# Kernel tuning notes

Hardware: AMD Instinct MI355X
Metric: run time of the kernel (lower is better)

## Reference

```python
import jax, jax.numpy as jnp
import numpy as np

N_NODES = 100_000
N_EDGES = 1_600_000
NUM_GRAPHS = 512
D1, D2, D3, D5, NUM_CLASSES = 3, 50, 15, 10, 6
BN_EPS = 1e-5


def setup_inputs() -> dict:
    key = jax.random.key(0)
    ks = jax.random.split(key, 16)

    def w(k, shape):
        fan_in = shape[0]
        return jax.random.normal(k, shape, jnp.float32) / np.sqrt(fan_in).astype(np.float32)

    return {
        "x": jax.random.normal(ks[0], (N_NODES, D1), jnp.float32),
        "edge_attr": jax.random.normal(ks[1], (N_EDGES, D1), jnp.float32),
        # edge MLP: Lin(9,50) -> ReLU -> Lin(50,15)
        "edge_w1": w(ks[2], (3 * D1, D2)), "edge_b1": jnp.zeros((D2,), jnp.float32),
        "edge_w2": w(ks[3], (D2, D3)), "edge_b2": jnp.zeros((D3,), jnp.float32),
        # node MLP: Lin(18,50) -> ReLU -> Lin(50,15)
        "node_w1": w(ks[4], (D1 + D3, D2)), "node_b1": jnp.zeros((D2,), jnp.float32),
        "node_w2": w(ks[5], (D2, D3)), "node_b2": jnp.zeros((D3,), jnp.float32),
        # readout head
        "fc1_w": w(ks[6], (D3, D5)), "fc1_b": jnp.zeros((D5,), jnp.float32),
        "bn_gamma": jnp.ones((D5,), jnp.float32), "bn_beta": jnp.zeros((D5,), jnp.float32),
        "fc2_w": w(ks[7], (D5, NUM_CLASSES)), "fc2_b": jnp.zeros((NUM_CLASSES,), jnp.float32),
        # graph structure
        "edge_index": jax.random.randint(ks[8], (2, N_EDGES), 0, N_NODES, jnp.int32),
        "batch": jnp.sort(jax.random.randint(ks[9], (N_NODES,), 0, NUM_GRAPHS, jnp.int32)),
    }


def _segment_mean(vals, idx, num_segments):
    s = jax.ops.segment_sum(vals, idx, num_segments=num_segments)
    c = jax.ops.segment_sum(jnp.ones((vals.shape[0], 1), vals.dtype), idx,
                            num_segments=num_segments)
    return s / jnp.maximum(c, 1.0)


def reference(x, edge_attr,
              edge_w1, edge_b1, edge_w2, edge_b2,
              node_w1, node_b1, node_w2, node_b2,
              fc1_w, fc1_b, bn_gamma, bn_beta, fc2_w, fc2_b,
              edge_index, batch):
    row, col = edge_index[0], edge_index[1]
    # edge model: cat([x[row], x[col], edge_attr]) -> MLP  -> [E, D3]
    e_in = jnp.concatenate([x[row], x[col], edge_attr], axis=1)
    edge_attr2 = jax.nn.relu(e_in @ edge_w1 + edge_b1) @ edge_w2 + edge_b2
    # node model: cat([x[col], edge_attr2]) -> MLP -> scatter_mean over row
    n_in = jnp.concatenate([x[col], edge_attr2], axis=1)  # [E, D1+D3]
    msg = jax.nn.relu(n_in @ node_w1 + node_b1) @ node_w2 + node_b2  # [E, D3]
    x2 = _segment_mean(msg, row, x.shape[0])  # [N, D3]
    # global mean pool per graph -> [G, D3]
    u = _segment_mean(x2, batch, NUM_GRAPHS)
    # head: fc1 -> BatchNorm1d (batch stats) -> relu -> fc2 -> log_softmax
    h = u @ fc1_w + fc1_b
    mu = h.mean(axis=0)
    var = h.var(axis=0)  # biased, matches BN training normalization
    h = bn_gamma * (h - mu) * jax.lax.rsqrt(var + BN_EPS) + bn_beta
    h = jax.nn.relu(h)
    logits = h @ fc2_w + fc2_b
    return jax.nn.log_softmax(logits, axis=1)
```

## Files before the change

### kernel.cpp

```cpp
#include <hip/hip_runtime.h>
#include <hip/hip_bf16.h>
#include <math.h>

#define N_NODES    100000
#define N_EDGES    1600000
#define NUM_GRAPHS 512
#define D2 50
#define D3 15
#define D5 10
#define NCLS 6
#define BN_EPS 1e-5f

#define NBLK1 ((N_NODES + 1023) / 1024)

#define W_EW1T 0
#define W_EW2T 2560
#define W_NW1T 3712
#define W_NW2T 6272
#define W_TOTAL 7680

#define S_EIN  40
#define S_HB   104
#define ACT_WAVE 2944

typedef __attribute__((ext_vector_type(8))) short short8;
typedef __attribute__((ext_vector_type(4))) float float4_;

__device__ __forceinline__ unsigned short f2bf(float f) {
    __hip_bfloat16 h = __float2bfloat16(f);
    union { __hip_bfloat16 h; unsigned short u; } c; c.h = h; return c.u;
}
__device__ __forceinline__ float bf2f(unsigned short u) {
    union { __hip_bfloat16 h; unsigned short u; } c; c.u = u;
    return __bfloat162float(c.h);
}
__device__ __forceinline__ unsigned int pkbf(float a, float b) {
    return (unsigned int)f2bf(a) | ((unsigned int)f2bf(b) << 16);
}

__global__ __launch_bounds__(256) void prep_kernel(
    const float* __restrict__ ew1, const float* __restrict__ eb1,
    const float* __restrict__ ew2, const float* __restrict__ eb2,
    const float* __restrict__ nw1, const float* __restrict__ nb1,
    const float* __restrict__ nw2, const float* __restrict__ nb2,
    unsigned short* __restrict__ wh, unsigned short* __restrict__ wl,
    const float* __restrict__ x, ushort4* __restrict__ x4b,
    const int* __restrict__ edge_index, int* __restrict__ counts)
{
    int gtid = blockIdx.x * 256 + threadIdx.x;
    int gsz = gridDim.x * 256;

    for (int i = gtid; i < W_TOTAL; i += gsz) {
        float v = 0.0f;
        if (i < W_EW2T) {
            int m = i / 40, k = i % 40;
            if (m < 50) {
                if (k < 3)                 v = ew1[k * 50 + m];
                else if (k == 3)           v = eb1[m];
                else if (k >= 4 && k < 7)  v = ew1[(k - 1) * 50 + m];
                else if (k >= 8 && k < 11) v = ew1[(k - 2) * 50 + m];
            }
        } else if (i < W_NW1T) {
            int j = i - W_EW2T; int m = j / 72, k = j % 72;
            if (m < 15) { if (k < 50) v = ew2[k * 15 + m]; else if (k == 50) v = eb2[m]; }
        } else if (i < W_NW2T) {
            int j = i - W_NW1T; int m = j / 40, k = j % 40;
            if (m < 50) {
                if (k < 15)                  v = nw1[(3 + k) * 50 + m];
                else if (k >= 16 && k < 19)  v = nw1[(k - 16) * 50 + m];
                else if (k == 19)            v = nb1[m];
            }
        } else if (i < 7424) {
            int j = i - W_NW2T; int m = j / 72, k = j % 72;
            if (m < 15) { if (k < 50) v = nw2[k * 15 + m]; else if (k == 50) v = nb2[m]; }
        }
        unsigned short h = f2bf(v);
        unsigned short l = f2bf(v - bf2f(h));
        wh[i] = h; wl[i] = l;
    }

    for (int n = gtid; n < N_NODES; n += gsz) {
        ushort4 v;
        v.x = f2bf(x[n * 3 + 0]); v.y = f2bf(x[n * 3 + 1]);
        v.z = f2bf(x[n * 3 + 2]); v.w = 0;
        x4b[n] = v;
    }

    for (int e = gtid; e < N_EDGES; e += gsz)
        atomicAdd(&counts[edge_index[e]], 1);
}

__global__ __launch_bounds__(1024) void scan1_kernel(
    const int* __restrict__ counts, int* __restrict__ scanned, int* __restrict__ bsums)
{
    __shared__ int tmp[1024];
    int i = blockIdx.x * 1024 + threadIdx.x;
    int v = (i < N_NODES) ? counts[i] : 0;
    tmp[threadIdx.x] = v;
    __syncthreads();
    #pragma unroll
    for (int off = 1; off < 1024; off <<= 1) {
        int t = (threadIdx.x >= off) ? tmp[threadIdx.x - off] : 0;
        __syncthreads();
        tmp[threadIdx.x] += t;
        __syncthreads();
    }
    int incl = tmp[threadIdx.x];
    if (i < N_NODES) scanned[i] = incl - v;
    if (threadIdx.x == 1023) bsums[blockIdx.x] = incl;
}

__global__ __launch_bounds__(128) void scan2_kernel(
    const int* __restrict__ bsums, int* __restrict__ bofs)
{
    __shared__ int tmp[128];
    int v = (threadIdx.x < NBLK1) ? bsums[threadIdx.x] : 0;
    tmp[threadIdx.x] = v;
    __syncthreads();
    #pragma unroll
    for (int off = 1; off < 128; off <<= 1) {
        int t = (threadIdx.x >= off) ? tmp[threadIdx.x - off] : 0;
        __syncthreads();
        tmp[threadIdx.x] += t;
        __syncthreads();
    }
    if (threadIdx.x < NBLK1) bofs[threadIdx.x] = tmp[threadIdx.x] - v;
}

__global__ __launch_bounds__(256) void scan3_kernel(
    const int* __restrict__ scanned, const int* __restrict__ bofs,
    int* __restrict__ cursor)
{
    int n = blockIdx.x * 256 + threadIdx.x;
    if (n >= N_NODES) return;
    cursor[n] = scanned[n] + bofs[n >> 10];
}

__global__ __launch_bounds__(256) void edge_mfma_kernel(
    const unsigned short* __restrict__ wh_g, const unsigned short* __restrict__ wl_g,
    const ushort4* __restrict__ x4b, const float* __restrict__ edge_attr,
    const int* __restrict__ edge_index,
    int* __restrict__ cursor, float* __restrict__ msg)
{
    __shared__ unsigned short act[4][ACT_WAVE];

    int tid = threadIdx.x, wave = tid >> 6, lane = tid & 63;
    int t16 = lane & 15, quad = lane >> 4;
    unsigned short* ein  = &act[wave][0];
    unsigned short* hbuf = &act[wave][640];
    unsigned short* h2in = &act[wave][2304];

    short8 A1h[4], A1l[4], A3h[4], A3l[4];
    #pragma unroll
    for (int t4 = 0; t4 < 4; t4++) {
        int o1 = W_EW1T + (t4 * 16 + t16) * 40 + quad * 8;
        A1h[t4] = *(const short8*)(wh_g + o1);
        A1l[t4] = *(const short8*)(wl_g + o1);
        int o3 = W_NW1T + (t4 * 16 + t16) * 40 + quad * 8;
        A3h[t4] = *(const short8*)(wh_g + o3);
        A3l[t4] = *(const short8*)(wl_g + o3);
    }
    short8 A2h[2], A2l[2], A4h[2], A4l[2];
    #pragma unroll
    for (int kc = 0; kc < 2; kc++) {
        int o2 = W_EW2T + t16 * 72 + kc * 32 + quad * 8;
        A2h[kc] = *(const short8*)(wh_g + o2);
        A2l[kc] = *(const short8*)(wl_g + o2);
        int o4 = W_NW2T + t16 * 72 + kc * 32 + quad * 8;
        A4h[kc] = *(const short8*)(wh_g + o4);
        A4l[kc] = *(const short8*)(wl_g + o4);
    }

    ushort4 z4; z4.x = 0; z4.y = 0; z4.z = 0; z4.w = 0;
    for (int i = lane; i < 16 * 5; i += 64) {
        int r = i / 5, c = i % 5;
        *(ushort4*)&ein[r * S_EIN + 12 + c * 4] = z4;
    }
    for (int i = lane; i < 16 * 3; i += 64) {
        int r = i / 3, c = i % 3;
        *(ushort4*)&h2in[r * S_EIN + 20 + c * 4] = z4;
    }
    __builtin_amdgcn_wave_barrier();

    int gw = blockIdx.x * 4 + wave;
    for (int t = gw; t < N_EDGES / 16; t += 4000) {
        int e = t * 16 + t16;
        int pos = 0;
        if (quad == 0) {
            int row = edge_index[e];
            ushort4 xr = x4b[row];
            ushort4 w; w.x = xr.x; w.y = xr.y; w.z = xr.z; w.w = 0x3F80;
            *(ushort4*)&ein[t16 * S_EIN + 0] = w;
            pos = atomicAdd(&cursor[row], 1);
        } else if (quad == 1) {
            int col = edge_index[N_EDGES + e];
            ushort4 xc = x4b[col];
            *(ushort4*)&ein[t16 * S_EIN + 4] = xc;
        } else if (quad == 2) {
            ushort4 w;
            w.x = f2bf(edge_attr[e * 3 + 0]);
            w.y = f2bf(edge_attr[e * 3 + 1]);
            w.z = f2bf(edge_attr[e * 3 + 2]);
            w.w = 0;
            *(ushort4*)&ein[t16 * S_EIN + 8] = w;
        } else {
            int col = edge_index[N_EDGES + e];
            ushort4 xc = x4b[col];
            ushort4 w; w.x = xc.x; w.y = xc.y; w.z = xc.z; w.w = 0x3F80;
            *(ushort4*)&h2in[t16 * S_EIN + 16] = w;
        }
        pos = __shfl(pos, t16);
        __builtin_amdgcn_wave_barrier();

        short8 B1 = *(short8*)&ein[t16 * S_EIN + quad * 8];
        #pragma unroll
        for (int t4 = 0; t4 < 4; t4++) {
            float4_ z = {0.f, 0.f, 0.f, 0.f};
            z = __builtin_amdgcn_mfma_f32_16x16x32_bf16(A1l[t4], B1, z, 0, 0, 0);
            z = __builtin_amdgcn_mfma_f32_16x16x32_bf16(A1h[t4], B1, z, 0, 0, 0);
            float r0 = fmaxf(z[0], 0.f), r1 = fmaxf(z[1], 0.f);
            float r2 = fmaxf(z[2], 0.f), r3 = fmaxf(z[3], 0.f);
            uint2 pk; pk.x = pkbf(r0, r1); pk.y = pkbf(r2, r3);
            *(uint2*)&hbuf[t16 * S_HB + t4 * 16 + quad * 4] = pk;
        }
        if (quad == 0) hbuf[t16 * S_HB + 50] = 0x3F80;
        __builtin_amdgcn_wave_barrier();

        float4_ acc2 = {0.f, 0.f, 0.f, 0.f};
        #pragma unroll
        for (int kc = 0; kc < 2; kc++) {
            short8 B = *(short8*)&hbuf[t16 * S_HB + kc * 32 + quad * 8];
            acc2 = __builtin_amdgcn_mfma_f32_16x16x32_bf16(A2l[kc], B, acc2, 0, 0, 0);
            acc2 = __builtin_amdgcn_mfma_f32_16x16x32_bf16(A2h[kc], B, acc2, 0, 0, 0);
        }
        {
            uint2 pk; pk.x = pkbf(acc2[0], acc2[1]); pk.y = pkbf(acc2[2], acc2[3]);
            *(uint2*)&h2in[t16 * S_EIN + quad * 4] = pk;
        }
        __builtin_amdgcn_wave_barrier();

        short8 B3 = *(short8*)&h2in[t16 * S_EIN + quad * 8];
        #pragma unroll
        for (int t4 = 0; t4 < 4; t4++) {
            float4_ z = {0.f, 0.f, 0.f, 0.f};
            z = __builtin_amdgcn_mfma_f32_16x16x32_bf16(A3l[t4], B3, z, 0, 0, 0);
            z = __builtin_amdgcn_mfma_f32_16x16x32_bf16(A3h[t4], B3, z, 0, 0, 0);
            float r0 = fmaxf(z[0], 0.f), r1 = fmaxf(z[1], 0.f);
            float r2 = fmaxf(z[2], 0.f), r3 = fmaxf(z[3], 0.f);
            uint2 pk; pk.x = pkbf(r0, r1); pk.y = pkbf(r2, r3);
            *(uint2*)&hbuf[t16 * S_HB + t4 * 16 + quad * 4] = pk;
        }
        if (quad == 0) hbuf[t16 * S_HB + 50] = 0x3F80;
        __builtin_amdgcn_wave_barrier();

        float4_ accm = {0.f, 0.f, 0.f, 0.f};
        #pragma unroll
        for (int kc = 0; kc < 2; kc++) {
            short8 B = *(short8*)&hbuf[t16 * S_HB + kc * 32 + quad * 8];
            accm = __builtin_amdgcn_mfma_f32_16x16x32_bf16(A4l[kc], B, accm, 0, 0, 0);
            accm = __builtin_amdgcn_mfma_f32_16x16x32_bf16(A4h[kc], B, accm, 0, 0, 0);
        }
        *(float4_*)(msg + (size_t)pos * 16 + quad * 4) = accm;
        __builtin_amdgcn_wave_barrier();
    }
}

__global__ __launch_bounds__(256) void gather_pool_kernel(
    const float* __restrict__ msg, const int* __restrict__ scanned,
    const int* __restrict__ bofs, const int* __restrict__ counts,
    const int* __restrict__ batch, float* __restrict__ gsum)
{
    __shared__ float acc[64 * 16];
    int n0 = blockIdx.x * 256;
    int n = n0 + threadIdx.x;

    float v[16];
    #pragma unroll
    for (int k = 0; k < 16; k++) v[k] = 0.0f;
    if (n < N_NODES) {
        int start = scanned[n] + bofs[n >> 10];
        int deg = counts[n];
        for (int j = 0; j < deg; j++) {
            const float4* mp = (const float4*)(msg + (size_t)(start + j) * 16);
            float4 b0 = mp[0], b1 = mp[1], b2 = mp[2], b3 = mp[3];
            v[0] += b0.x;  v[1] += b0.y;  v[2] += b0.z;  v[3] += b0.w;
            v[4] += b1.x;  v[5] += b1.y;  v[6] += b1.z;  v[7] += b1.w;
            v[8] += b2.x;  v[9] += b2.y;  v[10] += b2.z; v[11] += b2.w;
            v[12] += b3.x; v[13] += b3.y; v[14] += b3.z;
        }
        float inv = 1.0f / fmaxf((float)deg, 1.0f);
        #pragma unroll
        for (int k = 0; k < 15; k++) v[k] *= inv;
        v[15] = 1.0f;
    }

    int gmin = batch[n0];
    int gmax = batch[min(n0 + 255, N_NODES - 1)];
    int range = gmax - gmin + 1;
    if (range <= 64) {
        for (int t = threadIdx.x; t < range * 16; t += 256) acc[t] = 0.0f;
        __syncthreads();
        if (n < N_NODES) {
            int g = batch[n] - gmin;
            float* dst = &acc[g * 16];
            #pragma unroll
            for (int k = 0; k < 16; k++) atomicAdd(&dst[k], v[k]);
        }
        __syncthreads();
        for (int t = threadIdx.x; t < range * 16; t += 256) {
            float w = acc[t];
            if (w != 0.0f) atomicAdd(&gsum[(size_t)gmin * 16 + t], w);
        }
    } else {
        if (n < N_NODES) {
            int g = batch[n];
            float* dst = gsum + (size_t)g * 16;
            #pragma unroll
            for (int k = 0; k < 16; k++) atomicAdd(&dst[k], v[k]);
        }
    }
}

__global__ __launch_bounds__(512) void head_kernel(
    const float* __restrict__ gsum,
    const float* __restrict__ fc1w, const float* __restrict__ fc1b,
    const float* __restrict__ gamma, const float* __restrict__ beta,
    const float* __restrict__ fc2w, const float* __restrict__ fc2b,
    float* __restrict__ out)
{
    __shared__ float ssum[D5], ssq[D5], smu[D5], sistd[D5];
    int g = threadIdx.x;
    if (g < D5) { ssum[g] = 0.0f; ssq[g] = 0.0f; }
    __syncthreads();

    const float* src = gsum + (size_t)g * 16;
    float inv = 1.0f / fmaxf(src[15], 1.0f);
    float u[D3];
    #pragma unroll
    for (int k = 0; k < D3; k++) u[k] = src[k] * inv;

    float h[D5];
    #pragma unroll
    for (int c = 0; c < D5; c++) h[c] = fc1b[c];
    #pragma unroll
    for (int k = 0; k < D3; k++) {
        float v = u[k];
        #pragma unroll
        for (int c = 0; c < D5; c++) h[c] = fmaf(v, fc1w[k * D5 + c], h[c]);
    }

    int lane = threadIdx.x & 63;
    #pragma unroll
    for (int c = 0; c < D5; c++) {
        float v = h[c];
        float v2 = v * v;
        #pragma unroll
        for (int off = 32; off >= 1; off >>= 1) {
            v  += __shfl_xor(v,  off);
            v2 += __shfl_xor(v2, off);
        }
        if (lane == 0) { atomicAdd(&ssum[c], v); atomicAdd(&ssq[c], v2); }
    }
    __syncthreads();
    if (g < D5) {
        float mu = ssum[g] * (1.0f / NUM_GRAPHS);
        float var = ssq[g] * (1.0f / NUM_GRAPHS) - mu * mu;
        smu[g] = mu;
        sistd[g] = rsqrtf(var + BN_EPS);
    }
    __syncthreads();

    float hn[D5];
    #pragma unroll
    for (int c = 0; c < D5; c++) {
        float v = gamma[c] * (h[c] - smu[c]) * sistd[c] + beta[c];
        hn[c] = fmaxf(v, 0.0f);
    }

    float lg[NCLS];
    #pragma unroll
    for (int j = 0; j < NCLS; j++) lg[j] = fc2b[j];
    #pragma unroll
    for (int c = 0; c < D5; c++) {
        float v = hn[c];
        #pragma unroll
        for (int j = 0; j < NCLS; j++) lg[j] = fmaf(v, fc2w[c * NCLS + j], lg[j]);
    }

    float m = lg[0];
    #pragma unroll
    for (int j = 1; j < NCLS; j++) m = fmaxf(m, lg[j]);
    float se = 0.0f;
    #pragma unroll
    for (int j = 0; j < NCLS; j++) se += expf(lg[j] - m);
    float lse = logf(se);
    #pragma unroll
    for (int j = 0; j < NCLS; j++) out[g * NCLS + j] = lg[j] - m - lse;
}

extern "C" void kernel_launch(void* const* d_in, const int* in_sizes, int n_in,
                              void* d_out, int out_size, void* d_ws, size_t ws_size,
                              hipStream_t stream) {
    const float* x         = (const float*)d_in[0];
    const float* edge_attr = (const float*)d_in[1];
    const float* ew1  = (const float*)d_in[2];
    const float* eb1  = (const float*)d_in[3];
    const float* ew2  = (const float*)d_in[4];
    const float* eb2  = (const float*)d_in[5];
    const float* nw1  = (const float*)d_in[6];
    const float* nb1  = (const float*)d_in[7];
    const float* nw2  = (const float*)d_in[8];
    const float* nb2  = (const float*)d_in[9];
    const float* fc1w = (const float*)d_in[10];
    const float* fc1b = (const float*)d_in[11];
    const float* gamma= (const float*)d_in[12];
    const float* beta = (const float*)d_in[13];
    const float* fc2w = (const float*)d_in[14];
    const float* fc2b = (const float*)d_in[15];
    const int* edge_index = (const int*)d_in[16];
    const int* batch      = (const int*)d_in[17];

    char* p = (char*)d_ws;
    float* msg = (float*)p;            p += (size_t)N_EDGES * 16 * sizeof(float);
    int* counts  = (int*)p;            p += (size_t)N_NODES * sizeof(int);
    int* scanned = (int*)p;            p += (size_t)N_NODES * sizeof(int);
    int* cursor  = (int*)p;            p += (size_t)N_NODES * sizeof(int);
    int* bsums   = (int*)p;            p += 128 * sizeof(int);
    int* bofs    = (int*)p;            p += 128 * sizeof(int);
    ushort4* x4b = (ushort4*)p;        p += (size_t)N_NODES * sizeof(ushort4);
    float* gsum  = (float*)p;          p += (size_t)NUM_GRAPHS * 16 * sizeof(float);
    unsigned short* wh = (unsigned short*)p; p += W_TOTAL * sizeof(unsigned short);
    unsigned short* wl = (unsigned short*)p; p += W_TOTAL * sizeof(unsigned short);

    hipMemsetAsync(counts, 0, (size_t)N_NODES * sizeof(int), stream);
    hipMemsetAsync(gsum, 0, (size_t)NUM_GRAPHS * 16 * sizeof(float), stream);

    int egrid = (N_EDGES + 255) / 256;
    int ngrid = (N_NODES + 255) / 256;

    prep_kernel<<<egrid, 256, 0, stream>>>(
        ew1, eb1, ew2, eb2, nw1, nb1, nw2, nb2, wh, wl,
        x, x4b, edge_index, counts);
    scan1_kernel<<<NBLK1, 1024, 0, stream>>>(counts, scanned, bsums);
    scan2_kernel<<<1, 128, 0, stream>>>(bsums, bofs);
    scan3_kernel<<<ngrid, 256, 0, stream>>>(scanned, bofs, cursor);
    edge_mfma_kernel<<<1000, 256, 0, stream>>>(
        wh, wl, x4b, edge_attr, edge_index, cursor, msg);
    gather_pool_kernel<<<ngrid, 256, 0, stream>>>(
        msg, scanned, bofs, counts, batch, gsum);
    head_kernel<<<1, 512, 0, stream>>>(
        gsum, fc1w, fc1b, gamma, beta, fc2w, fc2b, (float*)d_out);
}
```

Baseline: 382.4 us.

## Software-pipeline edge loads and process two 16-edge tiles per wave iteration

The edge MLP kernel now handles two 16-edge tiles per iteration with double LDS buffers, interleaving independent MFMA chains so they can hide each other's latency. The gathers and cursor atomics for the next pair of tiles are issued before the current tiles' MFMA work, overlapping memory latency with compute. The grid grows from 1000 to 2500 blocks with a fixed iteration count (50000 tiles / 10000 waves = 5). LDS per block doubles and register pressure rises, which may lower occupancy.

```diff
diff --git a/kernel.cpp b/kernel.cpp
--- a/kernel.cpp
+++ b/kernel.cpp
@@ -21,7 +21,12 @@
 
 #define S_EIN  40
 #define S_HB   104
-#define ACT_WAVE 2944
+#define ACT_WAVE 5888
+
+#define EDGE_BLOCKS 2500
+#define EDGE_WAVES  (EDGE_BLOCKS * 4)
+#define TILES32     (N_EDGES / 32)
+#define EDGE_ITERS  (TILES32 / EDGE_WAVES)
 
 typedef __attribute__((ext_vector_type(8))) short short8;
 typedef __attribute__((ext_vector_type(4))) float float4_;
@@ -136,6 +141,38 @@
     cursor[n] = scanned[n] + bofs[n >> 10];
 }
 
+__device__ __forceinline__ void load_stage(int e, int quad,
+    const int* __restrict__ edge_index, const ushort4* __restrict__ x4b,
+    const float* __restrict__ edge_attr, int* __restrict__ cursor,
+    ushort4& w, int& pos)
+{
+    if (quad == 0) {
+        int row = edge_index[e];
+        ushort4 xr = x4b[row];
+        w.x = xr.x; w.y = xr.y; w.z = xr.z; w.w = 0x3F80;
+        pos = atomicAdd(&cursor[row], 1);
+    } else if (quad == 1) {
+        int col = edge_index[N_EDGES + e];
+        w = x4b[col];
+    } else if (quad == 2) {
+        w.x = f2bf(edge_attr[e * 3 + 0]);
+        w.y = f2bf(edge_attr[e * 3 + 1]);
+        w.z = f2bf(edge_attr[e * 3 + 2]);
+        w.w = 0;
+    } else {
+        int col = edge_index[N_EDGES + e];
+        ushort4 xc = x4b[col];
+        w.x = xc.x; w.y = xc.y; w.z = xc.z; w.w = 0x3F80;
+    }
+}
+
+__device__ __forceinline__ void write_stage(
+    unsigned short* ein, unsigned short* h2in, int t16, int quad, ushort4 w)
+{
+    if (quad < 3) *(ushort4*)&ein[t16 * S_EIN + quad * 4] = w;
+    else          *(ushort4*)&h2in[t16 * S_EIN + 16] = w;
+}
+
 __global__ __launch_bounds__(256) void edge_mfma_kernel(
     const unsigned short* __restrict__ wh_g, const unsigned short* __restrict__ wl_g,
     const ushort4* __restrict__ x4b, const float* __restrict__ edge_attr,
@@ -146,9 +183,13 @@
 
     int tid = threadIdx.x, wave = tid >> 6, lane = tid & 63;
     int t16 = lane & 15, quad = lane >> 4;
-    unsigned short* ein  = &act[wave][0];
-    unsigned short* hbuf = &act[wave][640];
-    unsigned short* h2in = &act[wave][2304];
+    unsigned short* base = act[wave];
+    unsigned short* einA = base;
+    unsigned short* einB = base + 640;
+    unsigned short* h2A  = base + 1280;
+    unsigned short* h2B  = base + 1920;
+    unsigned short* hbA  = base + 2560;
+    unsigned short* hbB  = base + 4224;
 
     short8 A1h[4], A1l[4], A3h[4], A3l[4];
     #pragma unroll
@@ -174,94 +215,116 @@
     ushort4 z4; z4.x = 0; z4.y = 0; z4.z = 0; z4.w = 0;
     for (int i = lane; i < 16 * 5; i += 64) {
         int r = i / 5, c = i % 5;
-        *(ushort4*)&ein[r * S_EIN + 12 + c * 4] = z4;
+        *(ushort4*)&einA[r * S_EIN + 12 + c * 4] = z4;
+        *(ushort4*)&einB[r * S_EIN + 12 + c * 4] = z4;
     }
     for (int i = lane; i < 16 * 3; i += 64) {
         int r = i / 3, c = i % 3;
-        *(ushort4*)&h2in[r * S_EIN + 20 + c * 4] = z4;
+        *(ushort4*)&h2A[r * S_EIN + 20 + c * 4] = z4;
+        *(ushort4*)&h2B[r * S_EIN + 20 + c * 4] = z4;
     }
     __builtin_amdgcn_wave_barrier();
 
     int gw = blockIdx.x * 4 + wave;
-    for (int t = gw; t < N_EDGES / 16; t += 4000) {
-        int e = t * 16 + t16;
-        int pos = 0;
+    int t = gw;
+    ushort4 wA, wB; int posA = 0, posB = 0;
+    load_stage(t * 32 + t16,      quad, edge_index, x4b, edge_attr, cursor, wA, posA);
+    load_stage(t * 32 + 16 + t16, quad, edge_index, x4b, edge_attr, cursor, wB, posB);
+
+    for (int it = 0; it < EDGE_ITERS; it++) {
+        write_stage(einA, h2A, t16, quad, wA);
+        write_stage(einB, h2B, t16, quad, wB);
+        int p0 = __shfl(posA, t16);
+        int p1 = __shfl(posB, t16);
+        __builtin_amdgcn_wave_barrier();
+
+        int tn = t + EDGE_WAVES;
+        ushort4 nA = z4, nB = z4; int nposA = 0, nposB = 0;
+        if (it + 1 < EDGE_ITERS) {
+            load_stage(tn * 32 + t16,      quad, edge_index, x4b, edge_attr, cursor, nA, nposA);
+            load_stage(tn * 32 + 16 + t16, quad, edge_index, x4b, edge_attr, cursor, nB, nposB);
+        }
+
+        short8 B1a = *(short8*)&einA[t16 * S_EIN + quad * 8];
+        short8 B1b = *(short8*)&einB[t16 * S_EIN + quad * 8];
+        #pragma unroll
+        for (int t4 = 0; t4 < 4; t4++) {
+            float4_ zA = {0.f, 0.f, 0.f, 0.f}, zB = {0.f, 0.f, 0.f, 0.f};
+            zA = __builtin_amdgcn_mfma_f32_16x16x32_bf16(A1l[t4], B1a, zA, 0, 0, 0);
+            zB = __builtin_amdgcn_mfma_f32_16x16x32_bf16(A1l[t4], B1b, zB, 0, 0, 0);
+            zA = __builtin_amdgcn_mfma_f32_16x16x32_bf16(A1h[t4], B1a, zA, 0, 0, 0);
+            zB = __builtin_amdgcn_mfma_f32_16x16x32_bf16(A1h[t4], B1b, zB, 0, 0, 0);
+            uint2 pA, pB;
+            pA.x = pkbf(fmaxf(zA[0], 0.f), fmaxf(zA[1], 0.f));
+            pA.y = pkbf(fmaxf(zA[2], 0.f), fmaxf(zA[3], 0.f));
+            pB.x = pkbf(fmaxf(zB[0], 0.f), fmaxf(zB[1], 0.f));
+            pB.y = pkbf(fmaxf(zB[2], 0.f), fmaxf(zB[3], 0.f));
+            *(uint2*)&hbA[t16 * S_HB + t4 * 16 + quad * 4] = pA;
+            *(uint2*)&hbB[t16 * S_HB + t4 * 16 + quad * 4] = pB;
+        }
         if (quad == 0) {
-            int row = edge_index[e];
-            ushort4 xr = x4b[row];
-            ushort4 w; w.x = xr.x; w.y = xr.y; w.z = xr.z; w.w = 0x3F80;
-            *(ushort4*)&ein[t16 * S_EIN + 0] = w;
-            pos = atomicAdd(&cursor[row], 1);
-        } else if (quad == 1) {
-            int col = edge_index[N_EDGES + e];
-            ushort4 xc = x4b[col];
-            *(ushort4*)&ein[t16 * S_EIN + 4] = xc;
-        } else if (quad == 2) {
-            ushort4 w;
-            w.x = f2bf(edge_attr[e * 3 + 0]);
-            w.y = f2bf(edge_attr[e * 3 + 1]);
-            w.z = f2bf(edge_attr[e * 3 + 2]);
-            w.w = 0;
-            *(ushort4*)&ein[t16 * S_EIN + 8] = w;
-        } else {
-            int col = edge_index[N_EDGES + e];
-            ushort4 xc = x4b[col];
-            ushort4 w; w.x = xc.x; w.y = xc.y; w.z = xc.z; w.w = 0x3F80;
-            *(ushort4*)&h2in[t16 * S_EIN + 16] = w;
-        }
-        pos = __shfl(pos, t16);
+            hbA[t16 * S_HB + 50] = 0x3F80;
+            hbB[t16 * S_HB + 50] = 0x3F80;
+        }
         __builtin_amdgcn_wave_barrier();
 
-        short8 B1 = *(short8*)&ein[t16 * S_EIN + quad * 8];
+        float4_ a2A = {0.f, 0.f, 0.f, 0.f}, a2B = {0.f, 0.f, 0.f, 0.f};
+        #pragma unroll
+        for (int kc = 0; kc < 2; kc++) {
+            short8 BA = *(short8*)&hbA[t16 * S_HB + kc * 32 + quad * 8];
+            short8 BB = *(short8*)&hbB[t16 * S_HB + kc * 32 + quad * 8];
+            a2A = __builtin_amdgcn_mfma_f32_16x16x32_bf16(A2l[kc], BA, a2A, 0, 0, 0);
+            a2B = __builtin_amdgcn_mfma_f32_16x16x32_bf16(A2l[kc], BB, a2B, 0, 0, 0);
+            a2A = __builtin_amdgcn_mfma_f32_16x16x32_bf16(A2h[kc], BA, a2A, 0, 0, 0);
+            a2B = __builtin_amdgcn_mfma_f32_16x16x32_bf16(A2h[kc], BB, a2B, 0, 0, 0);
+        }
+        {
+            uint2 pA, pB;
+            pA.x = pkbf(a2A[0], a2A[1]); pA.y = pkbf(a2A[2], a2A[3]);
+            pB.x = pkbf(a2B[0], a2B[1]); pB.y = pkbf(a2B[2], a2B[3]);
+            *(uint2*)&h2A[t16 * S_EIN + quad * 4] = pA;
+            *(uint2*)&h2B[t16 * S_EIN + quad * 4] = pB;
+        }
+        __builtin_amdgcn_wave_barrier();
+
+        short8 B3a = *(short8*)&h2A[t16 * S_EIN + quad * 8];
+        short8 B3b = *(short8*)&h2B[t16 * S_EIN + quad * 8];
         #pragma unroll
         for (int t4 = 0; t4 < 4; t4++) {
-            float4_ z = {0.f, 0.f, 0.f, 0.f};
-            z = __builtin_amdgcn_mfma_f32_16x16x32_bf16(A1l[t4], B1, z, 0, 0, 0);
-            z = __builtin_amdgcn_mfma_f32_16x16x32_bf16(A1h[t4], B1, z, 0, 0, 0);
-            float r0 = fmaxf(z[0], 0.f), r1 = fmaxf(z[1], 0.f);
-            float r2 = fmaxf(z[2], 0.f), r3 = fmaxf(z[3], 0.f);
-            uint2 pk; pk.x = pkbf(r0, r1); pk.y = pkbf(r2, r3);
-            *(uint2*)&hbuf[t16 * S_HB + t4 * 16 + quad * 4] = pk;
-        }
-        if (quad == 0) hbuf[t16 * S_HB + 50] = 0x3F80;
+            float4_ zA = {0.f, 0.f, 0.f, 0.f}, zB = {0.f, 0.f, 0.f, 0.f};
+            zA = __builtin_amdgcn_mfma_f32_16x16x32_bf16(A3l[t4], B3a, zA, 0, 0, 0);
+            zB = __builtin_amdgcn_mfma_f32_16x16x32_bf16(A3l[t4], B3b, zB, 0, 0, 0);
+            zA = __builtin_amdgcn_mfma_f32_16x16x32_bf16(A3h[t4], B3a, zA, 0, 0, 0);
+            zB = __builtin_amdgcn_mfma_f32_16x16x32_bf16(A3h[t4], B3b, zB, 0, 0, 0);
+            uint2 pA, pB;
+            pA.x = pkbf(fmaxf(zA[0], 0.f), fmaxf(zA[1], 0.f));
+            pA.y = pkbf(fmaxf(zA[2], 0.f), fmaxf(zA[3], 0.f));
+            pB.x = pkbf(fmaxf(zB[0], 0.f), fmaxf(zB[1], 0.f));
+            pB.y = pkbf(fmaxf(zB[2], 0.f), fmaxf(zB[3], 0.f));
+            *(uint2*)&hbA[t16 * S_HB + t4 * 16 + quad * 4] = pA;
+            *(uint2*)&hbB[t16 * S_HB + t4 * 16 + quad * 4] = pB;
+        }
+        if (quad == 0) {
+            hbA[t16 * S_HB + 50] = 0x3F80;
+            hbB[t16 * S_HB + 50] = 0x3F80;
+        }
         __builtin_amdgcn_wave_barrier();
 
-        float4_ acc2 = {0.f, 0.f, 0.f, 0.f};
+        float4_ mA = {0.f, 0.f, 0.f, 0.f}, mB = {0.f, 0.f, 0.f, 0.f};
         #pragma unroll
         for (int kc = 0; kc < 2; kc++) {
-            short8 B = *(short8*)&hbuf[t16 * S_HB + kc * 32 + quad * 8];
-            acc2 = __builtin_amdgcn_mfma_f32_16x16x32_bf16(A2l[kc], B, acc2, 0, 0, 0);
-            acc2 = __builtin_amdgcn_mfma_f32_16x16x32_bf16(A2h[kc], B, acc2, 0, 0, 0);
-        }
-        {
-            uint2 pk; pk.x = pkbf(acc2[0], acc2[1]); pk.y = pkbf(acc2[2], acc2[3]);
-            *(uint2*)&h2in[t16 * S_EIN + quad * 4] = pk;
-        }
+            short8 BA = *(short8*)&hbA[t16 * S_HB + kc * 32 + quad * 8];
+            short8 BB = *(short8*)&hbB[t16 * S_HB + kc * 32 + quad * 8];
+            mA = __builtin_amdgcn_mfma_f32_16x16x32_bf16(A4l[kc], BA, mA, 0, 0, 0);
+            mB = __builtin_amdgcn_mfma_f32_16x16x32_bf16(A4l[kc], BB, mB, 0, 0, 0);
+            mA = __builtin_amdgcn_mfma_f32_16x16x32_bf16(A4h[kc], BA, mA, 0, 0, 0);
+            mB = __builtin_amdgcn_mfma_f32_16x16x32_bf16(A4h[kc], BB, mB, 0, 0, 0);
+        }
+        *(float4_*)(msg + (size_t)p0 * 16 + quad * 4) = mA;
+        *(float4_*)(msg + (size_t)p1 * 16 + quad * 4) = mB;
         __builtin_amdgcn_wave_barrier();
 
-        short8 B3 = *(short8*)&h2in[t16 * S_EIN + quad * 8];
-        #pragma unroll
-        for (int t4 = 0; t4 < 4; t4++) {
-            float4_ z = {0.f, 0.f, 0.f, 0.f};
-            z = __builtin_amdgcn_mfma_f32_16x16x32_bf16(A3l[t4], B3, z, 0, 0, 0);
-            z = __builtin_amdgcn_mfma_f32_16x16x32_bf16(A3h[t4], B3, z, 0, 0, 0);
-            float r0 = fmaxf(z[0], 0.f), r1 = fmaxf(z[1], 0.f);
-            float r2 = fmaxf(z[2], 0.f), r3 = fmaxf(z[3], 0.f);
-            uint2 pk; pk.x = pkbf(r0, r1); pk.y = pkbf(r2, r3);
-            *(uint2*)&hbuf[t16 * S_HB + t4 * 16 + quad * 4] = pk;
-        }
-        if (quad == 0) hbuf[t16 * S_HB + 50] = 0x3F80;
-        __builtin_amdgcn_wave_barrier();
-
-        float4_ accm = {0.f, 0.f, 0.f, 0.f};
-        #pragma unroll
-        for (int kc = 0; kc < 2; kc++) {
-            short8 B = *(short8*)&hbuf[t16 * S_HB + kc * 32 + quad * 8];
-            accm = __builtin_amdgcn_mfma_f32_16x16x32_bf16(A4l[kc], B, accm, 0, 0, 0);
-            accm = __builtin_amdgcn_mfma_f32_16x16x32_bf16(A4h[kc], B, accm, 0, 0, 0);
-        }
-        *(float4_*)(msg + (size_t)pos * 16 + quad * 4) = accm;
-        __builtin_amdgcn_wave_barrier();
+        wA = nA; wB = nB; posA = nposA; posB = nposB; t = tn;
     }
 }
 
@@ -444,7 +507,7 @@
     scan1_kernel<<<NBLK1, 1024, 0, stream>>>(counts, scanned, bsums);
     scan2_kernel<<<1, 128, 0, stream>>>(bsums, bofs);
     scan3_kernel<<<ngrid, 256, 0, stream>>>(scanned, bofs, cursor);
-    edge_mfma_kernel<<<1000, 256, 0, stream>>>(
+    edge_mfma_kernel<<<EDGE_BLOCKS, 256, 0, stream>>>(
         wh, wl, x4b, edge_attr, edge_index, cursor, msg);
     gather_pool_kernel<<<ngrid, 256, 0, stream>>>(
         msg, scanned, bofs, counts, batch, gsum);
```

Result: faster. 358.0 us (-6.4%).

## Replace LDS staging with bpermute register shuffles, process two edge tiles with prefetch

Applied to the files above, without the earlier changes.

The edge MLP kernel no longer stages activations through shared memory. It moves MFMA outputs into B-operand layout with ds_bpermute cross-lane shuffles. Each wave now handles two 16-edge tiles per iteration, interleaving their MFMAs to hide latency, and software-prefetches the next iteration's gathers and cursor atomics. The grid grows to 2500 blocks so the 32-edge tiles divide evenly. This raises register pressure and adds many bpermute instructions, and the input encoding is packed differently, which could break correctness if the lane mapping is wrong.

```diff
diff --git a/kernel.cpp b/kernel.cpp
--- a/kernel.cpp
+++ b/kernel.cpp
@@ -19,12 +19,14 @@
 #define W_NW2T 6272
 #define W_TOTAL 7680
 
-#define S_EIN  40
-#define S_HB   104
-#define ACT_WAVE 2944
+#define EDGE_BLOCKS 2500
+#define EDGE_WAVES  (EDGE_BLOCKS * 4)
+#define TILES32     (N_EDGES / 32)
+#define EDGE_ITERS  (TILES32 / EDGE_WAVES)
 
 typedef __attribute__((ext_vector_type(8))) short short8;
 typedef __attribute__((ext_vector_type(4))) float float4_;
+union BU { unsigned u[4]; short8 s; };
 
 __device__ __forceinline__ unsigned short f2bf(float f) {
     __hip_bfloat16 h = __float2bfloat16(f);
@@ -36,6 +38,9 @@
 }
 __device__ __forceinline__ unsigned int pkbf(float a, float b) {
     return (unsigned int)f2bf(a) | ((unsigned int)f2bf(b) << 16);
+}
+__device__ __forceinline__ unsigned bp(int s4, unsigned v) {
+    return (unsigned)__builtin_amdgcn_ds_bpermute(s4, (int)v);
 }
 
 __global__ __launch_bounds__(256) void prep_kernel(
@@ -136,132 +141,210 @@
     cursor[n] = scanned[n] + bofs[n >> 10];
 }
 
+struct EIn { unsigned w0, w1, w2, w3, h0, h1; int pos; };
+
+__device__ __forceinline__ EIn load_in(int ebase, int n, int quad,
+    const int* __restrict__ edge_index, const ushort4* __restrict__ x4b,
+    const float* __restrict__ edge_attr, int* __restrict__ cursor)
+{
+    EIn r; r.w0 = r.w1 = r.w2 = r.w3 = 0; r.h0 = r.h1 = 0; r.pos = 0;
+    int e = ebase + n;
+    if (quad == 0) {
+        int row = edge_index[e];
+        int col = edge_index[N_EDGES + e];
+        ushort4 xr = x4b[row];
+        ushort4 xc = x4b[col];
+        r.w0 = (unsigned)xr.x | ((unsigned)xr.y << 16);
+        r.w1 = (unsigned)xr.z | (0x3F80u << 16);
+        r.w2 = (unsigned)xc.x | ((unsigned)xc.y << 16);
+        r.w3 = (unsigned)xc.z;
+        r.pos = atomicAdd(&cursor[row], 1);
+    } else if (quad == 1) {
+        r.w0 = pkbf(edge_attr[e * 3 + 0], edge_attr[e * 3 + 1]);
+        r.w1 = (unsigned)f2bf(edge_attr[e * 3 + 2]);
+    } else if (quad == 2) {
+        int col = edge_index[N_EDGES + e];
+        ushort4 xc = x4b[col];
+        r.h0 = (unsigned)xc.x | ((unsigned)xc.y << 16);
+        r.h1 = (unsigned)xc.z | (0x3F80u << 16);
+    }
+    return r;
+}
+
+__device__ __forceinline__ void perm64(const unsigned U[4][2], int s0, int s1, bool hi,
+                                       short8& Bc0, short8& Bc1)
+{
+    BU b0, b1;
+    {
+        unsigned a0 = bp(s0, U[0][0]), a1 = bp(s0, U[1][0]);
+        unsigned a2 = bp(s0, U[0][1]), a3 = bp(s0, U[1][1]);
+        unsigned a4 = bp(s1, U[0][0]), a5 = bp(s1, U[1][0]);
+        unsigned a6 = bp(s1, U[0][1]), a7 = bp(s1, U[1][1]);
+        b0.u[0] = hi ? a1 : a0;
+        b0.u[1] = hi ? a3 : a2;
+        b0.u[2] = hi ? a5 : a4;
+        b0.u[3] = hi ? a7 : a6;
+    }
+    {
+        unsigned a0 = bp(s0, U[2][0]), a1 = bp(s0, U[3][0]);
+        unsigned a2 = bp(s0, U[2][1]), a3 = bp(s0, U[3][1]);
+        unsigned a4 = bp(s1, U[2][0]), a5 = bp(s1, U[3][0]);
+        unsigned a6 = bp(s1, U[2][1]), a7 = bp(s1, U[3][1]);
+        b1.u[0] = hi ? a1 : a0;
+        b1.u[1] = hi ? a3 : a2;
+        b1.u[2] = hi ? a5 : a4;
+        b1.u[3] = hi ? a7 : a6;
+    }
+    Bc0 = b0.s; Bc1 = b1.s;
+}
+
+__device__ __forceinline__ short8 perm16(const unsigned U2[2], int s0, int s1,
+                                         int quad, unsigned h0, unsigned h1)
+{
+    BU d;
+    d.u[0] = bp(s0, U2[0]);
+    d.u[1] = bp(s0, U2[1]);
+    d.u[2] = bp(s1, U2[0]);
+    d.u[3] = bp(s1, U2[1]);
+    if (quad == 2) { d.u[0] = h0; d.u[1] = h1; d.u[2] = 0; d.u[3] = 0; }
+    else if (quad == 3) { d.u[0] = 0; d.u[1] = 0; d.u[2] = 0; d.u[3] = 0; }
+    return d.s;
+}
+
 __global__ __launch_bounds__(256) void edge_mfma_kernel(
     const unsigned short* __restrict__ wh_g, const unsigned short* __restrict__ wl_g,
     const ushort4* __restrict__ x4b, const float* __restrict__ edge_attr,
     const int* __restrict__ edge_index,
     int* __restrict__ cursor, float* __restrict__ msg)
 {
-    __shared__ unsigned short act[4][ACT_WAVE];
-
     int tid = threadIdx.x, wave = tid >> 6, lane = tid & 63;
-    int t16 = lane & 15, quad = lane >> 4;
-    unsigned short* ein  = &act[wave][0];
-    unsigned short* hbuf = &act[wave][640];
-    unsigned short* h2in = &act[wave][2304];
+    int n = lane & 15, quad = lane >> 4;
 
     short8 A1h[4], A1l[4], A3h[4], A3l[4];
     #pragma unroll
     for (int t4 = 0; t4 < 4; t4++) {
-        int o1 = W_EW1T + (t4 * 16 + t16) * 40 + quad * 8;
+        int o1 = W_EW1T + (t4 * 16 + n) * 40 + quad * 8;
         A1h[t4] = *(const short8*)(wh_g + o1);
         A1l[t4] = *(const short8*)(wl_g + o1);
-        int o3 = W_NW1T + (t4 * 16 + t16) * 40 + quad * 8;
+        int o3 = W_NW1T + (t4 * 16 + n) * 40 + quad * 8;
         A3h[t4] = *(const short8*)(wh_g + o3);
         A3l[t4] = *(const short8*)(wl_g + o3);
     }
     short8 A2h[2], A2l[2], A4h[2], A4l[2];
     #pragma unroll
     for (int kc = 0; kc < 2; kc++) {
-        int o2 = W_EW2T + t16 * 72 + kc * 32 + quad * 8;
+        int o2 = W_EW2T + n * 72 + kc * 32 + quad * 8;
         A2h[kc] = *(const short8*)(wh_g + o2);
         A2l[kc] = *(const short8*)(wl_g + o2);
-        int o4 = W_NW2T + t16 * 72 + kc * 32 + quad * 8;
+        int o4 = W_NW2T + n * 72 + kc * 32 + quad * 8;
         A4h[kc] = *(const short8*)(wh_g + o4);
         A4l[kc] = *(const short8*)(wl_g + o4);
     }
 
-    ushort4 z4; z4.x = 0; z4.y = 0; z4.z = 0; z4.w = 0;
-    for (int i = lane; i < 16 * 5; i += 64) {
-        int r = i / 5, c = i % 5;
-        *(ushort4*)&ein[r * S_EIN + 12 + c * 4] = z4;
-    }
-    for (int i = lane; i < 16 * 3; i += 64) {
-        int r = i / 3, c = i % 3;
-        *(ushort4*)&h2in[r * S_EIN + 20 + c * 4] = z4;
-    }
-    __builtin_amdgcn_wave_barrier();
-
-    int gw = blockIdx.x * 4 + wave;
-    for (int t = gw; t < N_EDGES / 16; t += 4000) {
-        int e = t * 16 + t16;
-        int pos = 0;
-        if (quad == 0) {
-            int row = edge_index[e];
-            ushort4 xr = x4b[row];
-            ushort4 w; w.x = xr.x; w.y = xr.y; w.z = xr.z; w.w = 0x3F80;
-            *(ushort4*)&ein[t16 * S_EIN + 0] = w;
-            pos = atomicAdd(&cursor[row], 1);
-        } else if (quad == 1) {
-            int col = edge_index[N_EDGES + e];
-            ushort4 xc = x4b[col];
-            *(ushort4*)&ein[t16 * S_EIN + 4] = xc;
-        } else if (quad == 2) {
-            ushort4 w;
-            w.x = f2bf(edge_attr[e * 3 + 0]);
-            w.y = f2bf(edge_attr[e * 3 + 1]);
-            w.z = f2bf(edge_attr[e * 3 + 2]);
-            w.w = 0;
-            *(ushort4*)&ein[t16 * S_EIN + 8] = w;
-        } else {
-            int col = edge_index[N_EDGES + e];
-            ushort4 xc = x4b[col];
-            ushort4 w; w.x = xc.x; w.y = xc.y; w.z = xc.z; w.w = 0x3F80;
-            *(ushort4*)&h2in[t16 * S_EIN + 16] = w;
-        }
-        pos = __shfl(pos, t16);
-        __builtin_amdgcn_wave_barrier();
-
-        short8 B1 = *(short8*)&ein[t16 * S_EIN + quad * 8];
+    int s0 = ((quad & 1) * 32 + n) * 4;
+    int s1 = s0 + 64;
+    bool hi = (quad & 2) != 0;
+
+    int t = blockIdx.x * 4 + wave;
+    EIn cur0 = load_in(t * 32,      n, quad, edge_index, x4b, edge_attr, cursor);
+    EIn cur1 = load_in(t * 32 + 16, n, quad, edge_index, x4b, edge_attr, cursor);
+
+    for (int it = 0; it < EDGE_ITERS; it++) {
+        int p0 = __shfl(cur0.pos, n);
+        int p1 = __shfl(cur1.pos, n);
+
+        int tn = t + EDGE_WAVES;
+        EIn nx0, nx1;
+        nx0.w0 = nx0.w1 = nx0.w2 = nx0.w3 = nx0.h0 = nx0.h1 = 0; nx0.pos = 0;
+        nx1 = nx0;
+        if (it + 1 < EDGE_ITERS) {
+            nx0 = load_in(tn * 32,      n, quad, edge_index, x4b, edge_attr, cursor);
+            nx1 = load_in(tn * 32 + 16, n, quad, edge_index, x4b, edge_attr, cursor);
+        }
+
+        BU t0, t1;
+        t0.u[0] = cur0.w0; t0.u[1] = cur0.w1; t0.u[2] = cur0.w2; t0.u[3] = cur0.w3;
+        t1.u[0] = cur1.w0; t1.u[1] = cur1.w1; t1.u[2] = cur1.w2; t1.u[3] = cur1.w3;
+        short8 B1a = t0.s, B1b = t1.s;
+
+        unsigned U1a[4][2], U1b[4][2];
         #pragma unroll
         for (int t4 = 0; t4 < 4; t4++) {
-            float4_ z = {0.f, 0.f, 0.f, 0.f};
-            z = __builtin_amdgcn_mfma_f32_16x16x32_bf16(A1l[t4], B1, z, 0, 0, 0);
-            z = __builtin_amdgcn_mfma_f32_16x16x32_bf16(A1h[t4], B1, z, 0, 0, 0);
-            float r0 = fmaxf(z[0], 0.f), r1 = fmaxf(z[1], 0.f);
-            float r2 = fmaxf(z[2], 0.f), r3 = fmaxf(z[3], 0.f);
-            uint2 pk; pk.x = pkbf(r0, r1); pk.y = pkbf(r2, r3);
-            *(uint2*)&hbuf[t16 * S_HB + t4 * 16 + quad * 4] = pk;
-        }
-        if (quad == 0) hbuf[t16 * S_HB + 50] = 0x3F80;
-        __builtin_amdgcn_wave_barrier();
-
-        float4_ acc2 = {0.f, 0.f, 0.f, 0.f};
-        #pragma unroll
-        for (int kc = 0; kc < 2; kc++) {
-            short8 B = *(short8*)&hbuf[t16 * S_HB + kc * 32 + quad * 8];
-            acc2 = __builtin_amdgcn_mfma_f32_16x16x32_bf16(A2l[kc], B, acc2, 0, 0, 0);
-            acc2 = __builtin_amdgcn_mfma_f32_16x16x32_bf16(A2h[kc], B, acc2, 0, 0, 0);
-        }
-        {
-            uint2 pk; pk.x = pkbf(acc2[0], acc2[1]); pk.y = pkbf(acc2[2], acc2[3]);
-            *(uint2*)&h2in[t16 * S_EIN + quad * 4] = pk;
-        }
-        __builtin_amdgcn_wave_barrier();
-
-        short8 B3 = *(short8*)&h2in[t16 * S_EIN + quad * 8];
+            float4_ za = {0.f, 0.f, 0.f, 0.f}, zb = {0.f, 0.f, 0.f, 0.f};
+            za = __builtin_amdgcn_mfma_f32_16x16x32_bf16(A1l[t4], B1a, za, 0, 0, 0);
+            zb = __builtin_amdgcn_mfma_f32_16x16x32_bf16(A1l[t4], B1b, zb, 0, 0, 0);
+            za = __builtin_amdgcn_mfma_f32_16x16x32_bf16(A1h[t4], B1a, za, 0, 0, 0);
+            zb = __builtin_amdgcn_mfma_f32_16x16x32_bf16(A1h[t4], B1b, zb, 0, 0, 0);
+            U1a[t4][0] = pkbf(fmaxf(za[0], 0.f), fmaxf(za[1], 0.f));
+            U1a[t4][1] = pkbf(fmaxf(za[2], 0.f), fmaxf(za[3], 0.f));
+            U1b[t4][0] = pkbf(fmaxf(zb[0], 0.f), fmaxf(zb[1], 0.f));
+            U1b[t4][1] = pkbf(fmaxf(zb[2], 0.f), fmaxf(zb[3], 0.f));
+        }
+
+        short8 B2a0, B2a1, B2b0, B2b1;
+        perm64(U1a, s0, s1, hi, B2a0, B2a1);
+        perm64(U1b, s0, s1, hi, B2b0, B2b1);
+        if (quad == 2) {
+            BU fa, fb; fa.s = B2a1; fb.s = B2b1;
+            fa.u[1] = (fa.u[1] & 0xFFFF0000u) | 0x3F80u;
+            fb.u[1] = (fb.u[1] & 0xFFFF0000u) | 0x3F80u;
+            B2a1 = fa.s; B2b1 = fb.s;
+        }
+
+        float4_ a2a = {0.f, 0.f, 0.f, 0.f}, a2b = {0.f, 0.f, 0.f, 0.f};
+        a2a = __builtin_amdgcn_mfma_f32_16x16x32_bf16(A2l[0], B2a0, a2a, 0, 0, 0);
+        a2b = __builtin_amdgcn_mfma_f32_16x16x32_bf16(A2l[0], B2b0, a2b, 0, 0, 0);
+        a2a = __builtin_amdgcn_mfma_f32_16x16x32_bf16(A2h[0], B2a0, a2a, 0, 0, 0);
+        a2b = __builtin_amdgcn_mfma_f32_16x16x32_bf16(A2h[0], B2b0, a2b, 0, 0, 0);
+        a2a = __builtin_amdgcn_mfma_f32_16x16x32_bf16(A2l[1], B2a1, a2a, 0, 0, 0);
+        a2b = __builtin_amdgcn_mfma_f32_16x16x32_bf16(A2l[1], B2b1, a2b, 0, 0, 0);
+        a2a = __builtin_amdgcn_mfma_f32_16x16x32_bf16(A2h[1], B2a1, a2a, 0, 0, 0);
+        a2b = __builtin_amdgcn_mfma_f32_16x16x32_bf16(A2h[1], B2b1, a2b, 0, 0, 0);
+
+        unsigned U2a[2] = { pkbf(a2a[0], a2a[1]), pkbf(a2a[2], a2a[3]) };
+        unsigned U2b[2] = { pkbf(a2b[0], a2b[1]), pkbf(a2b[2], a2b[3]) };
+
+        short8 B3a = perm16(U2a, s0, s1, quad, cur0.h0, cur0.h1);
+        short8 B3b = perm16(U2b, s0, s1, quad, cur1.h0, cur1.h1);
+
+        unsigned U3a[4][2], U3b[4][2];
         #pragma unroll
         for (int t4 = 0; t4 < 4; t4++) {
-            float4_ z = {0.f, 0.f, 0.f, 0.f};
-            z = __builtin_amdgcn_mfma_f32_16x16x32_bf16(A3l[t4], B3, z, 0, 0, 0);
-            z = __builtin_amdgcn_mfma_f32_16x16x32_bf16(A3h[t4], B3, z, 0, 0, 0);
-            float r0 = fmaxf(z[0], 0.f), r1 = fmaxf(z[1], 0.f);
-            float r2 = fmaxf(z[2], 0.f), r3 = fmaxf(z[3], 0.f);
-            uint2 pk; pk.x = pkbf(r0, r1); pk.y = pkbf(r2, r3);
-            *(uint2*)&hbuf[t16 * S_HB + t4 * 16 + quad * 4] = pk;
-        }
-        if (quad == 0) hbuf[t16 * S_HB + 50] = 0x3F80;
-        __builtin_amdgcn_wave_barrier();
-
-        float4_ accm = {0.f, 0.f, 0.f, 0.f};
-        #pragma unroll
-        for (int kc = 0; kc < 2; kc++) {
-            short8 B = *(short8*)&hbuf[t16 * S_HB + kc * 32 + quad * 8];
-            accm = __builtin_amdgcn_mfma_f32_16x16x32_bf16(A4l[kc], B, accm, 0, 0, 0);
-            accm = __builtin_amdgcn_mfma_f32_16x16x32_bf16(A4h[kc], B, accm, 0, 0, 0);
-        }
-        *(float4_*)(msg + (size_t)pos * 16 + quad * 4) = accm;
-        __builtin_amdgcn_wave_barrier();
+            float4_ za = {0.f, 0.f, 0.f, 0.f}, zb = {0.f, 0.f, 0.f, 0.f};
+            za = __builtin_amdgcn_mfma_f32_16x16x32_bf16(A3l[t4], B3a, za, 0, 0, 0);
+            zb = __builtin_amdgcn_mfma_f32_16x16x32_bf16(A3l[t4], B3b, zb, 0, 0, 0);
+            za = __builtin_amdgcn_mfma_f32_16x16x32_bf16(A3h[t4], B3a, za, 0, 0, 0);
+            zb = __builtin_amdgcn_mfma_f32_16x16x32_bf16(A3h[t4], B3b, zb, 0, 0, 0);
+            U3a[t4][0] = pkbf(fmaxf(za[0], 0.f), fmaxf(za[1], 0.f));
+            U3a[t4][1] = pkbf(fmaxf(za[2], 0.f), fmaxf(za[3], 0.f));
+            U3b[t4][0] = pkbf(fmaxf(zb[0], 0.f), fmaxf(zb[1], 0.f));
+            U3b[t4][1] = pkbf(fmaxf(zb[2], 0.f), fmaxf(zb[3], 0.f));
+        }
+
+        short8 B4a0, B4a1, B4b0, B4b1;
+        perm64(U3a, s0, s1, hi, B4a0, B4a1);
+        perm64(U3b, s0, s1, hi, B4b0, B4b1);
+        if (quad == 2) {
+            BU fa, fb; fa.s = B4a1; fb.s = B4b1;
+            fa.u[1] = (fa.u[1] & 0xFFFF0000u) | 0x3F80u;
+            fb.u[1] = (fb.u[1] & 0xFFFF0000u) | 0x3F80u;
+            B4a1 = fa.s; B4b1 = fb.s;
+        }
+
+        float4_ ma = {0.f, 0.f, 0.f, 0.f}, mb = {0.f, 0.f, 0.f, 0.f};
+        ma = __builtin_amdgcn_mfma_f32_16x16x32_bf16(A4l[0], B4a0, ma, 0, 0, 0);
+        mb = __builtin_amdgcn_mfma_f32_16x16x32_bf16(A4l[0], B4b0, mb, 0, 0, 0);
+        ma = __builtin_amdgcn_mfma_f32_16x16x32_bf16(A4h[0], B4a0, ma, 0, 0, 0);
+        mb = __builtin_amdgcn_mfma_f32_16x16x32_bf16(A4h[0], B4b0, mb, 0, 0, 0);
+        ma = __builtin_amdgcn_mfma_f32_16x16x32_bf16(A4l[1], B4a1, ma, 0, 0, 0);
+        mb = __builtin_amdgcn_mfma_f32_16x16x32_bf16(A4l[1], B4b1, mb, 0, 0, 0);
+        ma = __builtin_amdgcn_mfma_f32_16x16x32_bf16(A4h[1], B4a1, ma, 0, 0, 0);
+        mb = __builtin_amdgcn_mfma_f32_16x16x32_bf16(A4h[1], B4b1, mb, 0, 0, 0);
+
+        *(float4_*)(msg + (size_t)p0 * 16 + quad * 4) = ma;
+        *(float4_*)(msg + (size_t)p1 * 16 + quad * 4) = mb;
+
+        cur0 = nx0; cur1 = nx1; t = tn;
     }
 }
 
@@ -444,7 +527,7 @@
     scan1_kernel<<<NBLK1, 1024, 0, stream>>>(counts, scanned, bsums);
     scan2_kernel<<<1, 128, 0, stream>>>(bsums, bofs);
     scan3_kernel<<<ngrid, 256, 0, stream>>>(scanned, bofs, cursor);
-    edge_mfma_kernel<<<1000, 256, 0, stream>>>(
+    edge_mfma_kernel<<<EDGE_BLOCKS, 256, 0, stream>>>(
         wh, wl, x4b, edge_attr, edge_index, cursor, msg);
     gather_pool_kernel<<<ngrid, 256, 0, stream>>>(
         msg, scanned, bofs, counts, batch, gsum);
```

After: 354.5 us. 7.3% less time.
